# Kernel optimization log

Measured on AMD Instinct MI355X. Metric: run time of the kernel, lower is better.

Reference implementation:

```python
import jax, jax.numpy as jnp
import numpy as np

B, S, L, CIN = 8, 32, 128, 1024
C1, C2 = 512, 256            # conv1_channel, conv2_channel
D1, D2 = 512, 128            # deconv1_channel, deconv2_channel
CD, SIM = 300, 128           # concept_dim, similarity_dim
L4 = L // 4


def _conv1d(x, w, b, pad):
    # x: [N, Cin, L], w: [Cout, Cin, k] (PyTorch layout)
    y = jax.lax.conv_general_dilated(x, w, (1,), [(pad, pad)],
                                     dimension_numbers=('NCH', 'OIH', 'NCH'))
    return y + b[None, :, None]


def _maxpool2(x):
    return jax.lax.reduce_window(x, -jnp.inf, jax.lax.max, (1, 1, 2), (1, 1, 2), 'VALID')


def _deconv1d(x, w, b):
    # PyTorch ConvTranspose1d(kernel=4, stride=2, padding=1); w: [Cin, Cout, k]
    w2 = jnp.flip(w, -1).transpose(1, 0, 2)  # -> OIH
    y = jax.lax.conv_general_dilated(x, w2, (1,), [(2, 2)], lhs_dilation=(2,),
                                     dimension_numbers=('NCH', 'OIH', 'NCH'))
    return y + b[None, :, None]


def setup_inputs():
    ks = jax.random.split(jax.random.key(0), 32)
    g = lambda i, shape: jax.random.normal(ks[i], shape, jnp.float32) * 0.02
    return {
        'batch': jax.random.normal(ks[0], (B, S, L, CIN), jnp.float32),
        'concept1': jax.random.normal(ks[1], (B, CD), jnp.float32),
        'concept2': jax.random.normal(ks[2], (B, CD), jnp.float32),
        'seg_len': jax.random.randint(ks[3], (B, S), 1, L + 1),
        'conv1_w': g(4, (C1, CIN, 5)), 'conv1_b': g(5, (C1,)),
        'conv2_w': g(6, (C2, C1, 5)), 'conv2_b': g(7, (C2,)),
        'sa_wq': g(8, (C2, C2)), 'sa_bq': g(9, (C2,)),
        'sa_wk': g(10, (C2, C2)), 'sa_bk': g(11, (C2,)),
        'sa_v': g(12, (C2,)), 'sa_vb': g(13, ()),
        'ca_wq': g(14, (CD, C2)), 'ca_bq': g(15, (C2,)),
        'ca_wk': g(16, (C2, C2)), 'ca_bk': g(17, (C2,)),
        'ca_v': g(18, (C2,)), 'ca_vb': g(19, ()),
        'dc1_w': g(20, (4 * C2, D1, 4)), 'dc1_b': g(21, (D1,)),
        'dc2_w': g(22, (D1, D2, 4)), 'dc2_b': g(23, (D2,)),
        'sim1_w': g(24, (D2, SIM)),
        'sim2_w': g(25, (CD, SIM)),
        'mlp_w': g(26, (SIM,)), 'mlp_b': g(27, ()),
    }


def reference(batch, concept1, concept2, seg_len,
              conv1_w, conv1_b, conv2_w, conv2_b,
              sa_wq, sa_bq, sa_wk, sa_bk, sa_v, sa_vb,
              ca_wq, ca_bq, ca_wk, ca_bk, ca_v, ca_vb,
              dc1_w, dc1_b, dc2_w, dc2_b,
              sim1_w, sim2_w, mlp_w, mlp_b):
    N = B * S
    # conv stack: [N, CIN, L] -> [N, C2, L/4]
    x = batch.reshape(N, L, CIN).transpose(0, 2, 1)
    t = _maxpool2(_conv1d(x, conv1_w, conv1_b, 2))
    t = _maxpool2(_conv1d(t, conv2_w, conv2_b, 2))
    tmp2 = t.transpose(0, 2, 1)                       # [N, L4, C2]

    # vectorized length mask: mask[i,j,k] = k < ceil(seg_len/4)  <=>  seg_len > 4k
    mask = (seg_len[:, :, None] > 4 * jnp.arange(L4)).reshape(N, 1, L4)

    # self additive attention over pooled positions
    qp = tmp2 @ sa_wq + sa_bq                          # [N, L4, H]
    kp = tmp2 @ sa_wk + sa_bk                          # [N, L4, H]
    s = jnp.einsum('nqkh,h->nqk', jnp.tanh(qp[:, :, None, :] + kp[:, None, :, :]), sa_v) + sa_vb
    s = jnp.where(mask, s, -1e9)
    a = jax.nn.softmax(s, axis=-1)                     # [N, L4, L4]
    self_res = jnp.einsum('nqk,nkc->nqc', a, tmp2)     # [N, L4, C2]

    # concept attention (query identical across positions -> compute once)
    ckp = tmp2 @ ca_wk + ca_bk                         # [N, L4, H]

    def concept_attn(c):
        cq = jnp.repeat(c @ ca_wq + ca_bq, S, axis=0)  # [N, H]
        sc = jnp.einsum('nkh,h->nk', jnp.tanh(cq[:, None, :] + ckp), ca_v) + ca_vb
        sc = jnp.where(mask[:, 0, :], sc, -1e9)
        ac = jax.nn.softmax(sc, axis=-1)               # [N, L4]
        r = jnp.einsum('nk,nkc->nc', ac, tmp2)         # [N, C2]
        return jnp.broadcast_to(r[:, None, :], (N, L4, C2))

    c1_res = concept_attn(concept1)
    c2_res = concept_attn(concept2)

    ar = jnp.concatenate([tmp2, self_res, c1_res, c2_res], axis=-1)  # [N, L4, 4*C2]
    r = _deconv1d(ar.transpose(0, 2, 1), dc1_w, dc1_b)               # [N, D1, L/2]
    r = _deconv1d(r, dc2_w, dc2_b).transpose(0, 2, 1)                # [N, L, D2]
    r = r.reshape(B, S * L, D2)

    sim1 = r @ sim1_w                                                # [B, S*L, SIM]

    def score(c):
        cs = (c @ sim2_w)[:, None, :] * sim1
        return jax.nn.sigmoid(cs @ mlp_w + mlp_b).reshape(B, S, L)

    return score(concept1), score(concept2)
```

## Files before the change

kernel.cpp:

```cpp
#include <hip/hip_runtime.h>
#include <cstdint>

typedef __bf16 bf16;
typedef __bf16 bf16x8 __attribute__((ext_vector_type(8)));
typedef float f32x4 __attribute__((ext_vector_type(4)));
typedef __attribute__((address_space(3))) bf16 lds_bf16;

__device__ __forceinline__ void gload_lds16(const void* g, void* l) {
  __builtin_amdgcn_global_load_lds(
      (const __attribute__((address_space(1))) unsigned int*)g,
      (__attribute__((address_space(3))) unsigned int*)l, 16, 0, 0);
}

__device__ __forceinline__ bf16x8 ld_b128(const lds_bf16* p) {
  bf16x8 r;
  asm volatile("ds_read_b128 %0, %1" : "=v"(r) : "v"(p));
  return r;
}

__device__ __forceinline__ float tanh_fast(float x) {
  float ax = fabsf(x);
  float e = __expf(ax + ax);
  float t = 1.0f - 2.0f / (e + 1.0f);
  return x < 0.0f ? -t : t;
}

template<int MODE>
__global__ __launch_bounds__(256, 2) void gemm_tap(
    const bf16* __restrict__ A, const bf16* __restrict__ Bt,
    const float* __restrict__ bias, bf16* __restrict__ Out,
    const bf16* __restrict__ zp,
    int snA, int logP, int logCI, int shift0, int ntaps, int cbCount,
    int cbCI, int pairs, int Ktot, int COt, int snO,
    const float* __restrict__ uu, const float* __restrict__ mlpb,
    float* __restrict__ outF)
{
  __shared__ __align__(16) bf16 Ab[2][2][4096];
  __shared__ __align__(16) bf16 Bb[2][2][4096];
  (void)pairs;
  const int tid  = threadIdx.x;
  const int wave = tid >> 6, lane = tid & 63;
  const int wr = wave >> 1, wc = wave & 1;
  const int m0  = blockIdx.x << 7;
  const int co0 = blockIdx.y << 7;
  const int P     = 1 << logP;
  const int Pmask = P - 1;
  const int CI    = 1 << logCI;
  f32x4 acc[4][4] = {};

  const int rowL = tid >> 2;
  const int kg   = tid & 3;
  const int fOff = ((kg ^ ((rowL + (rowL >> 2)) & 3)) << 3);

  const int mA0 = m0 + rowL,      nA0 = mA0 >> logP, pA0v = mA0 & Pmask;
  const int mA1 = m0 + rowL + 64, nA1 = mA1 >> logP, pA1v = mA1 & Pmask;
  const bf16* baseA0 = A + nA0 * snA + fOff;
  const bf16* baseA1 = A + nA1 * snA + fOff;
  const bf16* baseB0 = Bt + (co0 + rowL) * Ktot + fOff;
  const bf16* baseB1 = Bt + (co0 + rowL + 64) * Ktot + fOff;
  const bf16* zsrc = zp + fOff;

  const int frow  = lane & 15;
  const int rdOff = (((lane >> 4) ^ ((frow + (frow >> 2)) & 3)) << 3);

  const int ksA = wave & 1, ksB = ksA ^ 1;

  const int kpc = cbCI >> 6;
  const int NT  = cbCount * ntaps * kpc;
  int s_kc = 0, s_tap = 0, s_cb = 0;

  auto stageTile = [&](int bfs) {
    int sh  = s_tap + shift0;
    int rA0 = pA0v + sh, rA1 = pA1v + sh;
    int ko  = s_cb * cbCI + (s_kc << 6);
    const bf16* pa0 = ((unsigned)rA0 < (unsigned)P) ? baseA0 + rA0 * CI + ko : zsrc;
    const bf16* pa1 = ((unsigned)rA1 < (unsigned)P) ? baseA1 + rA1 * CI + ko : zsrc;
    const bf16* pb0 = baseB0 + (s_cb * ntaps + s_tap) * cbCI + (s_kc << 6);
    const bf16* pb1 = baseB1 + (s_cb * ntaps + s_tap) * cbCI + (s_kc << 6);
    gload_lds16(pa0,      &Ab[bfs][0][wave * 512]);
    gload_lds16(pa0 + 32, &Ab[bfs][1][wave * 512]);
    gload_lds16(pa1,      &Ab[bfs][0][2048 + wave * 512]);
    gload_lds16(pa1 + 32, &Ab[bfs][1][2048 + wave * 512]);
    gload_lds16(pb0,      &Bb[bfs][0][wave * 512]);
    gload_lds16(pb0 + 32, &Bb[bfs][1][wave * 512]);
    gload_lds16(pb1,      &Bb[bfs][0][2048 + wave * 512]);
    gload_lds16(pb1 + 32, &Bb[bfs][1][2048 + wave * 512]);
    if (++s_kc == kpc) { s_kc = 0; if (++s_tap == ntaps) { s_tap = 0; ++s_cb; } }
  };

  stageTile(0);
  __syncthreads();

  bf16x8 a0[4], a1[4], b0f[4], b1f[4];

#pragma unroll 1
  for (int t = 0; t < NT; ++t) {
    const int buf = t & 1;
#pragma unroll
    for (int i = 0; i < 4; ++i)
      a0[i] = ld_b128((const lds_bf16*)&Ab[buf][ksA][((wr << 6) + (i << 4) + frow) * 32 + rdOff]);
#pragma unroll
    for (int j = 0; j < 4; ++j)
      b0f[j] = ld_b128((const lds_bf16*)&Bb[buf][ksA][((wc << 6) + (j << 4) + frow) * 32 + rdOff]);
    if (t + 1 < NT) stageTile(buf ^ 1);
#pragma unroll
    for (int i = 0; i < 4; ++i)
      a1[i] = ld_b128((const lds_bf16*)&Ab[buf][ksB][((wr << 6) + (i << 4) + frow) * 32 + rdOff]);
#pragma unroll
    for (int j = 0; j < 4; ++j)
      b1f[j] = ld_b128((const lds_bf16*)&Bb[buf][ksB][((wc << 6) + (j << 4) + frow) * 32 + rdOff]);
    asm volatile("s_waitcnt lgkmcnt(8)" ::: "memory");
    __builtin_amdgcn_sched_barrier(0);
    __builtin_amdgcn_s_setprio(1);
#pragma unroll
    for (int i = 0; i < 4; ++i)
#pragma unroll
      for (int j = 0; j < 4; ++j)
        acc[i][j] = __builtin_amdgcn_mfma_f32_16x16x32_bf16(a0[i], b0f[j], acc[i][j], 0, 0, 0);
    __builtin_amdgcn_s_setprio(0);
    asm volatile("s_waitcnt lgkmcnt(0)" ::: "memory");
    __builtin_amdgcn_sched_barrier(0);
    __builtin_amdgcn_s_setprio(1);
#pragma unroll
    for (int i = 0; i < 4; ++i)
#pragma unroll
      for (int j = 0; j < 4; ++j)
        acc[i][j] = __builtin_amdgcn_mfma_f32_16x16x32_bf16(a1[i], b1f[j], acc[i][j], 0, 0, 0);
    __builtin_amdgcn_s_setprio(0);
    __syncthreads();
  }

  const int colL = lane & 15;
  const int rq   = (lane >> 4) << 2;

  if (MODE == 2) {
    float* scr0 = (float*)&Ab[0][0][0];
    float* scr1 = (float*)&Bb[0][0][0];
    const int n = m0 >> logP;
    const int b = n >> 5;
    const float* u0 = uu + b * 128;
    const float* u1 = uu + 1024 + b * 128;
#pragma unroll
    for (int i = 0; i < 4; ++i) {
#pragma unroll
      for (int r = 0; r < 4; ++r) {
        int rowLcl = (wr << 6) + (i << 4) + rq + r;
        float p0 = 0.0f, p1 = 0.0f;
#pragma unroll
        for (int j = 0; j < 4; ++j) {
          int gco = (wc << 6) + (j << 4) + colL;
          float v = acc[i][j][r];
          p0 += v * u0[gco];
          p1 += v * u1[gco];
        }
        scr0[rowLcl * 32 + (wc << 4) + colL] = p0;
        scr1[rowLcl * 32 + (wc << 4) + colL] = p1;
      }
    }
    __syncthreads();
    {
      int rowLcl = tid >> 1, c = tid & 1;
      const float* s = c ? scr1 : scr0;
      float sum = 0.0f;
#pragma unroll
      for (int k = 0; k < 32; ++k) sum += s[rowLcl * 32 + k];
      float val = 1.0f / (1.0f + __expf(-(sum + mlpb[0])));
      outF[(c ? 32768 : 0) + m0 + rowLcl] = val;
    }
    return;
  }

#pragma unroll
  for (int i = 0; i < 4; ++i) {
    int m = m0 + (wr << 6) + (i << 4) + rq;
    int n = m >> logP, p = m & Pmask;
#pragma unroll
    for (int j = 0; j < 4; ++j) {
      int gco = co0 + (wc << 6) + (j << 4) + colL;
      float bv = bias[gco];
      if (MODE == 1) {
        float v0 = fmaxf(acc[i][j][0], acc[i][j][1]) + bv;
        float v1 = fmaxf(acc[i][j][2], acc[i][j][3]) + bv;
        bf16* o = Out + n * snO + (p >> 1) * COt + gco;
        o[0]   = (bf16)v0;
        o[COt] = (bf16)v1;
      } else {
#pragma unroll
        for (int r = 0; r < 4; ++r)
          Out[n * snO + (p + r) * COt + gco] = (bf16)(acc[i][j][r] + bv);
      }
    }
  }
}

template<int LOGP, int LOGCI, int SH0, int NTAPS, int CBCNT, int CBCI>
__global__ __launch_bounds__(512, 2) void gemm8_pool(
    const bf16* __restrict__ A, const bf16* __restrict__ Bt,
    const float* __restrict__ bias, bf16* __restrict__ Out,
    const bf16* __restrict__ zp, int snA, int Ktot, int COt, int snO)
{
  __shared__ __align__(16) bf16 Ab[2][2][8192];
  __shared__ __align__(16) bf16 Bb[2][2][8192];
  constexpr int P = 1 << LOGP, CI = 1 << LOGCI;
  constexpr int KPC = CBCI / 64;
  constexpr int NT = CBCNT * NTAPS * KPC;

  const int tid = threadIdx.x;
  const int wave = tid >> 6, lane = tid & 63;
  const int wr = wave >> 2, wc = wave & 3;
  const int m0 = blockIdx.x << 8, co0 = blockIdx.y << 8;
  const int n0 = m0 >> LOGP;

  f32x4 acc[8][4] = {};

  const int rowP = tid >> 2;
  const int kOff = (((tid & 3) ^ ((rowP + (rowP >> 2)) & 3)) << 3);
  const bf16* baseA = A + n0 * snA + kOff;
  const bf16* pBs   = Bt + (co0 + rowP) * Ktot + kOff;
  const bf16* zsrc  = zp + kOff;
  const int ldsW = wave << 9;
  const int bStride = 128 * Ktot;

  const int frow = lane & 15;
  const int rdOff = (((lane >> 4) ^ ((frow + (frow >> 2)) & 3)) << 3);

  const int ksA = wave & 1, ksB = ksA ^ 1;

  int s_kc = 0, s_tap = 0, s_cb = 0;

  auto stageTile = [&](int bfs) {
    int rA = rowP + s_tap + SH0;
    bool v = (unsigned)rA < (unsigned)P;
    const bf16* pA0 = v ? baseA + rA * CI + (s_cb * CBCI + s_kc * 64) : zsrc;
    const bf16* pA1 = v ? pA0 + snA : zsrc;
    gload_lds16(pA0,      &Ab[bfs][0][ldsW]);
    gload_lds16(pA0 + 32, &Ab[bfs][1][ldsW]);
    gload_lds16(pA1,      &Ab[bfs][0][ldsW + 4096]);
    gload_lds16(pA1 + 32, &Ab[bfs][1][ldsW + 4096]);
    gload_lds16(pBs,                &Bb[bfs][0][ldsW]);
    gload_lds16(pBs + 32,           &Bb[bfs][1][ldsW]);
    gload_lds16(pBs + bStride,      &Bb[bfs][0][ldsW + 4096]);
    gload_lds16(pBs + bStride + 32, &Bb[bfs][1][ldsW + 4096]);
    pBs += 64;
    if (++s_kc == KPC) { s_kc = 0; if (++s_tap == NTAPS) { s_tap = 0; ++s_cb; } }
  };

  auto ldA = [&](int buf, int ks, int mh, int i) {
    return ld_b128((const lds_bf16*)
        &Ab[buf][ks][((wr << 7) + (mh << 6) + (i << 4) + frow) * 32 + rdOff]);
  };
  auto ldB = [&](int buf, int ks, int j) {
    return ld_b128((const lds_bf16*)
        &Bb[buf][ks][((wc << 6) + (j << 4) + frow) * 32 + rdOff]);
  };

  stageTile(0);
  __syncthreads();

  bf16x8 a0[4], a1[4], b0[4], b1[4];

#pragma unroll 1
  for (int t = 0; t < NT; ++t) {
    const int buf = t & 1;
#pragma unroll
    for (int i = 0; i < 4; ++i) a0[i] = ldA(buf, ksA, 0, i);
#pragma unroll
    for (int j = 0; j < 4; ++j) b0[j] = ldB(buf, ksA, j);
    if (t + 1 < NT) stageTile(buf ^ 1);
#pragma unroll
    for (int i = 0; i < 4; ++i) a1[i] = ldA(buf, ksA, 1, i);
    asm volatile("s_waitcnt lgkmcnt(4)" ::: "memory");
    __builtin_amdgcn_sched_barrier(0);
    __builtin_amdgcn_s_setprio(1);
#pragma unroll
    for (int i = 0; i < 4; ++i)
#pragma unroll
      for (int j = 0; j < 4; ++j)
        acc[i][j] = __builtin_amdgcn_mfma_f32_16x16x32_bf16(a0[i], b0[j], acc[i][j], 0, 0, 0);
    __builtin_amdgcn_s_setprio(0);
#pragma unroll
    for (int i = 0; i < 4; ++i) a0[i] = ldA(buf, ksB, 0, i);
#pragma unroll
    for (int j = 0; j < 4; ++j) b1[j] = ldB(buf, ksB, j);
    asm volatile("s_waitcnt lgkmcnt(8)" ::: "memory");
    __builtin_amdgcn_sched_barrier(0);
    __builtin_amdgcn_s_setprio(1);
#pragma unroll
    for (int i = 0; i < 4; ++i)
#pragma unroll
      for (int j = 0; j < 4; ++j)
        acc[4 + i][j] = __builtin_amdgcn_mfma_f32_16x16x32_bf16(a1[i], b0[j], acc[4 + i][j], 0, 0, 0);
    __builtin_amdgcn_s_setprio(0);
#pragma unroll
    for (int i = 0; i < 4; ++i) a1[i] = ldA(buf, ksB, 1, i);
    asm volatile("s_waitcnt lgkmcnt(4)" ::: "memory");
    __builtin_amdgcn_sched_barrier(0);
    __builtin_amdgcn_s_setprio(1);
#pragma unroll
    for (int i = 0; i < 4; ++i)
#pragma unroll
      for (int j = 0; j < 4; ++j)
        acc[i][j] = __builtin_amdgcn_mfma_f32_16x16x32_bf16(a0[i], b1[j], acc[i][j], 0, 0, 0);
    __builtin_amdgcn_s_setprio(0);
    asm volatile("s_waitcnt lgkmcnt(0)" ::: "memory");
    __builtin_amdgcn_sched_barrier(0);
    __builtin_amdgcn_s_setprio(1);
#pragma unroll
    for (int i = 0; i < 4; ++i)
#pragma unroll
      for (int j = 0; j < 4; ++j)
        acc[4 + i][j] = __builtin_amdgcn_mfma_f32_16x16x32_bf16(a1[i], b1[j], acc[4 + i][j], 0, 0, 0);
    __builtin_amdgcn_s_setprio(0);
    __syncthreads();
  }

  const int colL = lane & 15, rq = (lane >> 4) << 2;
#pragma unroll
  for (int i = 0; i < 8; ++i) {
    int m = m0 + (wr << 7) + (i << 4) + rq;
    int n = m >> LOGP, p = m & (P - 1);
    bf16* orow = Out + n * snO + (p >> 1) * COt;
#pragma unroll
    for (int j = 0; j < 4; ++j) {
      int gco = co0 + (wc << 6) + (j << 4) + colL;
      float bv = bias[gco];
      orow[gco]       = (bf16)(fmaxf(acc[i][j][0], acc[i][j][1]) + bv);
      orow[COt + gco] = (bf16)(fmaxf(acc[i][j][2], acc[i][j][3]) + bv);
    }
  }
}

__global__ __launch_bounds__(256) void prep_all(
    const float* __restrict__ conv1_w, const float* __restrict__ conv2_w,
    const float* __restrict__ sa_wq, const float* __restrict__ sa_wk,
    const float* __restrict__ ca_wk, const float* __restrict__ dc1_w,
    const float* __restrict__ dc2_w, const float* __restrict__ sim1_w,
    const float* __restrict__ c1b, const float* __restrict__ c2b,
    const float* __restrict__ sabq, const float* __restrict__ sabk,
    const float* __restrict__ cabk, const float* __restrict__ d1b,
    const float* __restrict__ d2b,
    const float* __restrict__ c1, const float* __restrict__ c2,
    const float* __restrict__ ca_wq, const float* __restrict__ ca_bq,
    const float* __restrict__ sim2_w, const float* __restrict__ mlp_w,
    const float* __restrict__ batch, bf16* __restrict__ bb16,
    bf16* __restrict__ Bt1, bf16* __restrict__ Bt2, bf16* __restrict__ Bqkc,
    bf16* __restrict__ Btd1, bf16* __restrict__ Btd2, bf16* __restrict__ Bts1,
    float* __restrict__ bias, float* __restrict__ cq, float* __restrict__ uu)
{
  const int blk = blockIdx.x;
  if (blk >= 27492) {
    int idx = ((blk - 27492) * 256 + threadIdx.x) * 8;
    float4 a = *(const float4*)&batch[idx];
    float4 b = *(const float4*)&batch[idx + 4];
    bf16x8 v;
    v[0] = (bf16)a.x; v[1] = (bf16)a.y; v[2] = (bf16)a.z; v[3] = (bf16)a.w;
    v[4] = (bf16)b.x; v[5] = (bf16)b.y; v[6] = (bf16)b.z; v[7] = (bf16)b.w;
    *(bf16x8*)&bb16[idx] = v;
    return;
  }
  if (blk < 27468) {
    int idx = blk * 256 + threadIdx.x;
    if (idx < 3072) {
      if (idx < 2944) {
        float v;
        if (idx < 512)       v = c1b[idx];
        else if (idx < 768)  v = c2b[idx - 512];
        else if (idx < 1024) v = sabq[idx - 768];
        else if (idx < 1280) v = sabk[idx - 1024];
        else if (idx < 1536) v = cabk[idx - 1280];
        else if (idx < 2560) v = d1b[(idx - 1536) & 511];
        else if (idx < 2816) v = d2b[(idx - 2560) & 127];
        else                 v = 0.0f;
        bias[idx] = v;
      }
    } else if (idx < 2624512) {
      int i = idx - 3072;
      int co = i / 5120, r = i - co * 5120;
      int cb = r / 1280, r2 = r - cb * 1280;
      int tap = r2 >> 8, cl = r2 & 255;
      Bt1[i] = (bf16)conv1_w[co * 5120 + (cb * 256 + cl) * 5 + tap];
    } else if (idx < 3279872) {
      int i = idx - 2624512;
      int co = i / 2560, r = i - co * 2560;
      int cb = r / 1280, r2 = r - cb * 1280;
      int tap = r2 >> 8, cl = r2 & 255;
      Bt2[i] = (bf16)conv2_w[co * 2560 + (cb * 256 + cl) * 5 + tap];
    } else if (idx < 3476480) {
      int i = idx - 3279872;
      int co = i >> 8, ci = i & 255;
      float v;
      if (co < 256)      v = sa_wq[ci * 256 + co];
      else if (co < 512) v = sa_wk[ci * 256 + (co - 256)];
      else               v = ca_wk[ci * 256 + (co - 512)];
      Bqkc[i] = (bf16)v;
    } else if (idx < 6622208) {
      int i = idx - 3476480;
      int co = i / 3072, r = i - co * 3072;
      int cb = r / 768, r2 = r - cb * 768;
      int tap = r2 >> 8, cl = r2 & 255;
      int ci = cb * 256 + cl;
      int par = co >> 9, c = co & 511;
      int ki = -1;
      if (par == 0) { if (tap == 1) ki = 1; else if (tap == 0) ki = 3; }
      else          { if (tap == 2) ki = 0; else if (tap == 1) ki = 2; }
      Btd1[i] = (ki >= 0) ? (bf16)dc1_w[ci * 2048 + c * 4 + ki] : (bf16)0.0f;
    } else if (idx < 7015424) {
      int i = idx - 6622208;
      int co = i / 1536, r = i - co * 1536;
      int cb = r / 768, r2 = r - cb * 768;
      int tap = r2 >> 8, cl = r2 & 255;
      int ci = cb * 256 + cl;
      int par = co >> 7, c = co & 127;
      int ki = -1;
      if (par == 0) { if (tap == 1) ki = 1; else if (tap == 0) ki = 3; }
      else          { if (tap == 2) ki = 0; else if (tap == 1) ki = 2; }
      Btd2[i] = (ki >= 0) ? (bf16)dc2_w[ci * 512 + c * 4 + ki] : (bf16)0.0f;
    } else {
      int i = idx - 7015424;
      int co = i >> 7, ci = i & 127;
      Bts1[i] = (bf16)sim1_w[ci * 128 + co];
    }
  } else {
    int sub = blk - 27468;
    if (sub < 16) {
      int o = sub * 256 + threadIdx.x;
      int c = o >> 11, b = (o >> 8) & 7, h = o & 255;
      const float* cc = (c ? c2 : c1) + b * 300;
      float acc = ca_bq[h];
      for (int j = 0; j < 300; ++j)
        acc += cc[j] * ca_wq[j * 256 + h];
      cq[o] = acc;
    } else {
      int o = (sub - 16) * 256 + threadIdx.x;
      int c = o >> 10, b = (o >> 7) & 7, m = o & 127;
      const float* cc = (c ? c2 : c1) + b * 300;
      float acc = 0.0f;
      for (int j = 0; j < 300; ++j)
        acc += cc[j] * sim2_w[j * 128 + m];
      uu[o] = acc * mlp_w[m];
    }
  }
}

__global__ __launch_bounds__(256) void kattn(
    const bf16* __restrict__ tmp2, const bf16* __restrict__ qkc,
    const float* __restrict__ sa_v, const float* __restrict__ sa_vb,
    const float* __restrict__ ca_v, const float* __restrict__ ca_vb,
    const float* __restrict__ cq, const int* __restrict__ seg,
    bf16* __restrict__ ar)
{
  const int n = blockIdx.x, tid = threadIdx.x;
  __shared__ __align__(16) bf16 t2[32 * 264];
  __shared__ __align__(16) bf16 bufA[32 * 264];
  __shared__ __align__(16) bf16 bufB[32 * 264];
  __shared__ float sv_s[256], cv_s[256];
  __shared__ float sbc[66];
  __shared__ float sbs[32 * 33];
  const int sl = seg[n];

#pragma unroll
  for (int rr = 0; rr < 4; ++rr) {
    int q = tid + (rr << 8);
    int k = q >> 5, c8 = (q & 31) << 3;
    *(uint4*)&t2[k * 264 + c8]   = *(const uint4*)&tmp2[n * 8192 + k * 256 + c8];
    *(uint4*)&bufA[k * 264 + c8] = *(const uint4*)&qkc[n * 24576 + k * 768 + 512 + c8];
  }
  sv_s[tid] = sa_v[tid];
  cv_s[tid] = ca_v[tid];
  __syncthreads();

  if (tid < 64) {
    int c = tid >> 5, k = tid & 31;
    const float* cqr = cq + (c * 8 + (n >> 5)) * 256;
    float acc = 0.0f;
    for (int h = 0; h < 256; ++h)
      acc += tanh_fast(cqr[h] + (float)bufA[k * 264 + h]) * cv_s[h];
    float sc = acc + ca_vb[0];
    sbc[c * 33 + k] = (sl > (k << 2)) ? sc : -1e9f;
  }
  __syncthreads();

#pragma unroll
  for (int rr = 0; rr < 4; ++rr) {
    int q = tid + (rr << 8);
    int k = q >> 5, c8 = (q & 31) << 3;
    *(uint4*)&bufB[k * 264 + c8] = *(const uint4*)&qkc[n * 24576 + k * 768 + c8];
    *(uint4*)&bufA[k * 264 + c8] = *(const uint4*)&qkc[n * 24576 + k * 768 + 256 + c8];
  }
  if (tid < 2) {
    float* row = &sbc[tid * 33];
    float mx = -1e30f;
    for (int k = 0; k < 32; ++k) mx = fmaxf(mx, row[k]);
    float sum = 0.0f;
    for (int k = 0; k < 32; ++k) { float e = __expf(row[k] - mx); row[k] = e; sum += e; }
    float inv = 1.0f / sum;
    for (int k = 0; k < 32; ++k) row[k] *= inv;
  }
  __syncthreads();

  {
    int col = tid;
    float rr0 = 0.0f, rr1 = 0.0f;
    for (int k = 0; k < 32; ++k) {
      float tv = (float)t2[k * 264 + col];
      rr0 += sbc[k] * tv;
      rr1 += sbc[33 + k] * tv;
    }
    bf16 b0 = (bf16)rr0, b1 = (bf16)rr1;
    bf16* arn = ar + n * 32768;
    for (int q = 0; q < 32; ++q) {
      arn[q * 1024 + col]       = t2[q * 264 + col];
      arn[q * 1024 + 512 + col] = b0;
      arn[q * 1024 + 768 + col] = b1;
    }
  }
  {
    float svb = sa_vb[0];
#pragma unroll
    for (int rr = 0; rr < 4; ++rr) {
      int id = tid + (rr << 8);
      int q = id >> 5, k = id & 31;
      float acc = 0.0f;
      for (int h = 0; h < 256; ++h)
        acc += tanh_fast((float)bufB[q * 264 + h] + (float)bufA[k * 264 + h]) * sv_s[h];
      float sc = acc + svb;
      sbs[q * 33 + k] = (sl > (k << 2)) ? sc : -1e9f;
    }
  }
  __syncthreads();

  if (tid < 32) {
    float* row = &sbs[tid * 33];
    float mx = -1e30f;
    for (int k = 0; k < 32; ++k) mx = fmaxf(mx, row[k]);
    float sum = 0.0f;
    for (int k = 0; k < 32; ++k) { float e = __expf(row[k] - mx); row[k] = e; sum += e; }
    float inv = 1.0f / sum;
    for (int k = 0; k < 32; ++k) row[k] *= inv;
  }
  __syncthreads();

  {
    int col = tid;
    bf16* arn = ar + n * 32768;
    for (int q = 0; q < 32; ++q) {
      float acc = 0.0f;
      for (int k = 0; k < 32; ++k)
        acc += sbs[q * 33 + k] * (float)t2[k * 264 + col];
      arn[q * 1024 + 256 + col] = (bf16)acc;
    }
  }
}

extern "C" void kernel_launch(void* const* d_in, const int* in_sizes, int n_in,
                              void* d_out, int out_size, void* d_ws, size_t ws_size,
                              hipStream_t stream) {
  const float* batch    = (const float*)d_in[0];
  const float* concept1 = (const float*)d_in[1];
  const float* concept2 = (const float*)d_in[2];
  const int*   seg      = (const int*)d_in[3];
  const float* conv1_w  = (const float*)d_in[4];
  const float* conv1_b  = (const float*)d_in[5];
  const float* conv2_w  = (const float*)d_in[6];
  const float* conv2_b  = (const float*)d_in[7];
  const float* sa_wq    = (const float*)d_in[8];
  const float* sa_bq    = (const float*)d_in[9];
  const float* sa_wk    = (const float*)d_in[10];
  const float* sa_bk    = (const float*)d_in[11];
  const float* sa_v     = (const float*)d_in[12];
  const float* sa_vb    = (const float*)d_in[13];
  const float* ca_wq    = (const float*)d_in[14];
  const float* ca_bq    = (const float*)d_in[15];
  const float* ca_wk    = (const float*)d_in[16];
  const float* ca_bk    = (const float*)d_in[17];
  const float* ca_v     = (const float*)d_in[18];
  const float* ca_vb    = (const float*)d_in[19];
  const float* dc1_w    = (const float*)d_in[20];
  const float* dc1_b    = (const float*)d_in[21];
  const float* dc2_w    = (const float*)d_in[22];
  const float* dc2_b    = (const float*)d_in[23];
  const float* sim1_w   = (const float*)d_in[24];
  const float* sim2_w   = (const float*)d_in[25];
  const float* mlp_w    = (const float*)d_in[26];
  const float* mlp_b    = (const float*)d_in[27];

  char* ws = (char*)d_ws;
  bf16* bb16  = (bf16*)(ws + 0);
  bf16* qkcb  = (bf16*)(ws + 0);
  bf16* arb   = (bf16*)(ws + 12582912);
  bf16* d1    = (bf16*)(ws + 29360128);
  bf16* rbuf  = (bf16*)(ws + 46137344);
  bf16* t1    = (bf16*)(ws + 67108864);
  bf16* tmp2b = (bf16*)(ws + 83886080);
  bf16* Bt1   = (bf16*)(ws + 88080384);
  bf16* Bt2   = (bf16*)(ws + 93323264);
  bf16* Bqkc  = (bf16*)(ws + 94633984);
  bf16* Btd1  = (bf16*)(ws + 95027200);
  bf16* Btd2  = (bf16*)(ws + 101318656);
  bf16* Bts1  = (bf16*)(ws + 102105088);
  float* biasall = (float*)(ws + 102137856);
  float* cqb  = (float*)(ws + 102149632);
  float* uub  = (float*)(ws + 102166016);
  const bf16* zp = (const bf16*)(biasall + 2816);
  float* outp = (float*)d_out;

  prep_all<<<43876, 256, 0, stream>>>(
      conv1_w, conv2_w, sa_wq, sa_wk, ca_wk, dc1_w, dc2_w, sim1_w,
      conv1_b, conv2_b, sa_bq, sa_bk, ca_bk, dc1_b, dc2_b,
      concept1, concept2, ca_wq, ca_bq, sim2_w, mlp_w,
      batch, bb16,
      Bt1, Bt2, Bqkc, Btd1, Btd2, Bts1, biasall, cqb, uub);

  gemm8_pool<7, 10, -2, 5, 4, 256><<<dim3(128, 2), 512, 0, stream>>>(
      bb16, Bt1, biasall + 0, t1, zp, 131072, 5120, 512, 32768);

  gemm_tap<1><<<dim3(128, 2), 256, 0, stream>>>(
      t1, Bt2, biasall + 512, tmp2b, zp, 32768, 6, 9, -2, 5, 2, 256, 4, 2560, 256, 8192,
      nullptr, nullptr, nullptr);

  gemm_tap<0><<<dim3(64, 6), 256, 0, stream>>>(
      tmp2b, Bqkc, biasall + 768, qkcb, zp, 8192, 5, 8, 0, 1, 1, 256, 4, 256, 768, 24576,
      nullptr, nullptr, nullptr);

  kattn<<<256, 256, 0, stream>>>(tmp2b, qkcb, sa_v, sa_vb, ca_v, ca_vb, cqb, seg, arb);

  gemm_tap<0><<<dim3(64, 8), 256, 0, stream>>>(
      arb, Btd1, biasall + 1536, d1, zp, 32768, 5, 10, -1, 3, 4, 256, 4, 3072, 1024, 32768,
      nullptr, nullptr, nullptr);

  gemm_tap<0><<<dim3(128, 2), 256, 0, stream>>>(
      d1, Btd2, biasall + 2560, rbuf, zp, 32768, 6, 9, -1, 3, 2, 256, 4, 1536, 256, 16384,
      nullptr, nullptr, nullptr);

  gemm_tap<2><<<dim3(256, 1), 256, 0, stream>>>(
      rbuf, Bts1, biasall + 2816, nullptr, zp, 16384, 7, 7, 0, 1, 1, 128, 2, 128, 128, 16384,
      uub, mlp_b, outp);
}
```

Baseline: 617.1 us.

## Load conv GEMM weight fragments directly from global into registers, bypassing LDS

The pooled conv GEMM kernel no longer stages the B (weight) tile through shared memory. Each lane now loads its own B fragments from global memory straight into registers, prefetching the next k-step's fragments between MFMA groups. This halves LDS usage and drops the B-side LDS writes and reads, which should improve occupancy and cut LDS bandwidth pressure. In exchange, each wave re-reads weights from global or L2 with no reuse across waves, and the global loads may stall the MFMA stream because the s_waitcnt lgkmcnt(0) barriers do not cover vmcnt.

After: 689.5 us. 1.12x slower.

```diff
diff --git a/kernel.cpp b/kernel.cpp
--- a/kernel.cpp
+++ b/kernel.cpp
@@ -200,7 +200,6 @@
     const bf16* __restrict__ zp, int snA, int Ktot, int COt, int snO)
 {
   __shared__ __align__(16) bf16 Ab[2][2][8192];
-  __shared__ __align__(16) bf16 Bb[2][2][8192];
   constexpr int P = 1 << LOGP, CI = 1 << LOGCI;
   constexpr int KPC = CBCI / 64;
   constexpr int NT = CBCNT * NTAPS * KPC;
@@ -216,15 +215,14 @@
   const int rowP = tid >> 2;
   const int kOff = (((tid & 3) ^ ((rowP + (rowP >> 2)) & 3)) << 3);
   const bf16* baseA = A + n0 * snA + kOff;
-  const bf16* pBs   = Bt + (co0 + rowP) * Ktot + kOff;
   const bf16* zsrc  = zp + kOff;
   const int ldsW = wave << 9;
-  const int bStride = 128 * Ktot;
 
   const int frow = lane & 15;
   const int rdOff = (((lane >> 4) ^ ((frow + (frow >> 2)) & 3)) << 3);
 
-  const int ksA = wave & 1, ksB = ksA ^ 1;
+  const bf16* pBbase = Bt + (co0 + (wc << 6) + frow) * Ktot + ((lane >> 4) << 3);
+  const int jstep = 16 * Ktot;
 
   int s_kc = 0, s_tap = 0, s_cb = 0;
 
@@ -237,11 +235,6 @@
     gload_lds16(pA0 + 32, &Ab[bfs][1][ldsW]);
     gload_lds16(pA1,      &Ab[bfs][0][ldsW + 4096]);
     gload_lds16(pA1 + 32, &Ab[bfs][1][ldsW + 4096]);
-    gload_lds16(pBs,                &Bb[bfs][0][ldsW]);
-    gload_lds16(pBs + 32,           &Bb[bfs][1][ldsW]);
-    gload_lds16(pBs + bStride,      &Bb[bfs][0][ldsW + 4096]);
-    gload_lds16(pBs + bStride + 32, &Bb[bfs][1][ldsW + 4096]);
-    pBs += 64;
     if (++s_kc == KPC) { s_kc = 0; if (++s_tap == NTAPS) { s_tap = 0; ++s_cb; } }
   };
 
@@ -249,59 +242,30 @@
     return ld_b128((const lds_bf16*)
         &Ab[buf][ks][((wr << 7) + (mh << 6) + (i << 4) + frow) * 32 + rdOff]);
   };
-  auto ldB = [&](int buf, int ks, int j) {
-    return ld_b128((const lds_bf16*)
-        &Bb[buf][ks][((wc << 6) + (j << 4) + frow) * 32 + rdOff]);
-  };
-
+
+  bf16x8 b[8];
+  {
+    const bf16* p = pBbase;
+#pragma unroll
+    for (int j = 0; j < 4; ++j) {
+      b[j]     = *(const bf16x8*)(p);
+      b[4 + j] = *(const bf16x8*)(p + 32);
+      p += jstep;
+    }
+  }
   stageTile(0);
   __syncthreads();
 
-  bf16x8 a0[4], a1[4], b0[4], b1[4];
+  bf16x8 a[4];
+  int bu = 64;
 
 #pragma unroll 1
   for (int t = 0; t < NT; ++t) {
     const int buf = t & 1;
-#pragma unroll
-    for (int i = 0; i < 4; ++i) a0[i] = ldA(buf, ksA, 0, i);
-#pragma unroll
-    for (int j = 0; j < 4; ++j) b0[j] = ldB(buf, ksA, j);
-    if (t + 1 < NT) stageTile(buf ^ 1);
-#pragma unroll
-    for (int i = 0; i < 4; ++i) a1[i] = ldA(buf, ksA, 1, i);
-    asm volatile("s_waitcnt lgkmcnt(4)" ::: "memory");
-    __builtin_amdgcn_sched_barrier(0);
-    __builtin_amdgcn_s_setprio(1);
-#pragma unroll
-    for (int i = 0; i < 4; ++i)
-#pragma unroll
-      for (int j = 0; j < 4; ++j)
-        acc[i][j] = __builtin_amdgcn_mfma_f32_16x16x32_bf16(a0[i], b0[j], acc[i][j], 0, 0, 0);
-    __builtin_amdgcn_s_setprio(0);
-#pragma unroll
-    for (int i = 0; i < 4; ++i) a0[i] = ldA(buf, ksB, 0, i);
-#pragma unroll
-    for (int j = 0; j < 4; ++j) b1[j] = ldB(buf, ksB, j);
-    asm volatile("s_waitcnt lgkmcnt(8)" ::: "memory");
-    __builtin_amdgcn_sched_barrier(0);
-    __builtin_amdgcn_s_setprio(1);
-#pragma unroll
-    for (int i = 0; i < 4; ++i)
-#pragma unroll
-      for (int j = 0; j < 4; ++j)
-        acc[4 + i][j] = __builtin_amdgcn_mfma_f32_16x16x32_bf16(a1[i], b0[j], acc[4 + i][j], 0, 0, 0);
-    __builtin_amdgcn_s_setprio(0);
-#pragma unroll
-    for (int i = 0; i < 4; ++i) a1[i] = ldA(buf, ksB, 1, i);
-    asm volatile("s_waitcnt lgkmcnt(4)" ::: "memory");
-    __builtin_amdgcn_sched_barrier(0);
-    __builtin_amdgcn_s_setprio(1);
-#pragma unroll
-    for (int i = 0; i < 4; ++i)
-#pragma unroll
-      for (int j = 0; j < 4; ++j)
-        acc[i][j] = __builtin_amdgcn_mfma_f32_16x16x32_bf16(a0[i], b1[j], acc[i][j], 0, 0, 0);
-    __builtin_amdgcn_s_setprio(0);
+    const bool pre = (t + 1 < NT);
+#pragma unroll
+    for (int i = 0; i < 4; ++i) a[i] = ldA(buf, 0, 0, i);
+    if (pre) stageTile(buf ^ 1);
     asm volatile("s_waitcnt lgkmcnt(0)" ::: "memory");
     __builtin_amdgcn_sched_barrier(0);
     __builtin_amdgcn_s_setprio(1);
@@ -309,8 +273,52 @@
     for (int i = 0; i < 4; ++i)
 #pragma unroll
       for (int j = 0; j < 4; ++j)
-        acc[4 + i][j] = __builtin_amdgcn_mfma_f32_16x16x32_bf16(a1[i], b1[j], acc[4 + i][j], 0, 0, 0);
+        acc[i][j] = __builtin_amdgcn_mfma_f32_16x16x32_bf16(a[i], b[j], acc[i][j], 0, 0, 0);
     __builtin_amdgcn_s_setprio(0);
+#pragma unroll
+    for (int i = 0; i < 4; ++i) a[i] = ldA(buf, 0, 1, i);
+    asm volatile("s_waitcnt lgkmcnt(0)" ::: "memory");
+    __builtin_amdgcn_sched_barrier(0);
+    __builtin_amdgcn_s_setprio(1);
+#pragma unroll
+    for (int i = 0; i < 4; ++i)
+#pragma unroll
+      for (int j = 0; j < 4; ++j)
+        acc[4 + i][j] = __builtin_amdgcn_mfma_f32_16x16x32_bf16(a[i], b[j], acc[4 + i][j], 0, 0, 0);
+    __builtin_amdgcn_s_setprio(0);
+    if (pre) {
+      const bf16* p = pBbase + bu;
+#pragma unroll
+      for (int j = 0; j < 4; ++j) { b[j] = *(const bf16x8*)(p); p += jstep; }
+    }
+#pragma unroll
+    for (int i = 0; i < 4; ++i) a[i] = ldA(buf, 1, 0, i);
+    asm volatile("s_waitcnt lgkmcnt(0)" ::: "memory");
+    __builtin_amdgcn_sched_barrier(0);
+    __builtin_amdgcn_s_setprio(1);
+#pragma unroll
+    for (int i = 0; i < 4; ++i)
+#pragma unroll
+      for (int j = 0; j < 4; ++j)
+        acc[i][j] = __builtin_amdgcn_mfma_f32_16x16x32_bf16(a[i], b[4 + j], acc[i][j], 0, 0, 0);
+    __builtin_amdgcn_s_setprio(0);
+#pragma unroll
+    for (int i = 0; i < 4; ++i) a[i] = ldA(buf, 1, 1, i);
+    asm volatile("s_waitcnt lgkmcnt(0)" ::: "memory");
+    __builtin_amdgcn_sched_barrier(0);
+    __builtin_amdgcn_s_setprio(1);
+#pragma unroll
+    for (int i = 0; i < 4; ++i)
+#pragma unroll
+      for (int j = 0; j < 4; ++j)
+        acc[4 + i][j] = __builtin_amdgcn_mfma_f32_16x16x32_bf16(a[i], b[4 + j], acc[4 + i][j], 0, 0, 0);
+    __builtin_amdgcn_s_setprio(0);
+    if (pre) {
+      const bf16* p = pBbase + bu + 32;
+#pragma unroll
+      for (int j = 0; j < 4; ++j) { b[4 + j] = *(const bf16x8*)(p); p += jstep; }
+      bu += 64;
+    }
     __syncthreads();
   }
 
```
